# Performance work log

Hardware: AMD Instinct MI355X
Metric: run time of the kernel (lower is better)

The kernel has to match this reference:

```python
import jax, jax.numpy as jnp
import numpy as np

N_NODES = 100000
N_EDGES = 1600000
N_GRAPHS = 64
D_IN = 128
D_HID = 128
D_OUT = 4
LEAKY_SLOPE = 0.01  # nn.LeakyReLU default


def setup_inputs() -> dict:
    key = jax.random.key(0)
    k1, k2, k3, k4, k5 = jax.random.split(key, 5)
    x = jax.random.normal(k1, (N_NODES, D_IN), dtype=jnp.float32)
    edge_index = jax.random.randint(k2, (2, N_EDGES), 0, N_NODES, dtype=jnp.int32)
    batch = jnp.sort(jax.random.randint(k3, (N_NODES,), 0, N_GRAPHS, dtype=jnp.int32))
    s1 = 1.0 / np.sqrt(D_IN)
    W1 = jax.random.uniform(k4, (D_IN, D_HID), jnp.float32, -s1, s1)
    b1 = jnp.zeros((D_HID,), jnp.float32)
    W2 = jax.random.uniform(k5, (D_HID, D_OUT), jnp.float32, -s1, s1)
    b2 = jnp.zeros((D_OUT,), jnp.float32)
    return {"x": x, "edge_index": edge_index, "batch": batch,
            "W1": W1, "b1": b1, "W2": W2, "b2": b2}


def _gcn_conv(x, src, dst, norm, W, b, n_nodes):
    # h = X W; messages = norm * h[src]; aggregate at dst; add bias
    h = x @ W
    msg = h[src] * norm[:, None]
    agg = jax.ops.segment_sum(msg, dst, num_segments=n_nodes)
    return agg + b


def reference(x, edge_index, batch, W1, b1, W2, b2):
    n = x.shape[0]
    # add self-loops (PyG GCNConv default)
    loops = jnp.arange(n, dtype=edge_index.dtype)
    src = jnp.concatenate([edge_index[0], loops])
    dst = jnp.concatenate([edge_index[1], loops])
    # symmetric normalization: deg over target index, weight 1
    deg = jax.ops.segment_sum(jnp.ones_like(src, dtype=x.dtype), dst, num_segments=n)
    deg_is = jnp.where(deg > 0, jax.lax.rsqrt(deg), 0.0)
    norm = deg_is[src] * deg_is[dst]

    h = _gcn_conv(x, src, dst, norm, W1, b1, n)
    h = jnp.where(h >= 0, h, LEAKY_SLOPE * h)  # LeakyReLU
    # dropout is identity at inference
    h = _gcn_conv(h, src, dst, norm, W2, b2, n)

    # global mean pool over graphs
    sums = jax.ops.segment_sum(h, batch, num_segments=N_GRAPHS)
    cnts = jax.ops.segment_sum(jnp.ones((n,), h.dtype), batch, num_segments=N_GRAPHS)
    pooled = sums / jnp.maximum(cnts, 1.0)[:, None]
    return jax.nn.softmax(pooled, axis=1)
```

## Files before the change

### kernel.cpp

```cpp
#include <hip/hip_runtime.h>

#define D 128
#define NG 64
#define NPB 256
#define MAXBK 512
#define CAPB 8192
#define PCHUNK 4096
#define PLCAP 5376
#define ENTCAP 21
#define LDA 136

typedef unsigned int uint;
typedef unsigned short ushort_t;
typedef unsigned char uchar_t;
typedef float v2f __attribute__((ext_vector_type(2)));
typedef short s8v __attribute__((ext_vector_type(8)));
typedef float f4v __attribute__((ext_vector_type(4)));

__device__ __forceinline__ uint bfr(float x) {
    uint u = __float_as_uint(x);
    return (u + 0x7FFFu + ((u >> 16) & 1u)) >> 16;
}

__global__ __launch_bounds__(256) void k_init(const float* __restrict__ W,
                                              short* __restrict__ W1T,
                                              int* __restrict__ gcur,
                                              float* __restrict__ psum,
                                              float* __restrict__ pcnt, int NBK) {
    int tid = threadIdx.x;
    int idx = blockIdx.x * 256 + tid;
    int nn = idx >> 7, kk = idx & 127;
    W1T[idx] = (short)bfr(W[kk * D + nn]);
    if (idx < NBK) gcur[idx] = idx * CAPB;
    if (blockIdx.x == 0) {
        psum[tid] = 0.f;
        if (tid < NG) pcnt[tid] = 0.f;
    }
}

__global__ __launch_bounds__(256) void k_part(const int* __restrict__ edge,
                                              int* __restrict__ gcur, int* __restrict__ p1,
                                              int E, int NBK) {
    __shared__ int hist[MAXBK], scn[MAXBK], curb[MAXBK], fixb[MAXBK];
    __shared__ int ps[256];
    __shared__ int sortb[PCHUNK];
    __shared__ ushort_t sbkt[PCHUNK];
    int tid = threadIdx.x;
    for (int i = tid; i < MAXBK; i += 256) { hist[i] = 0; curb[i] = 0; }
    __syncthreads();
    int lo = blockIdx.x * PCHUNK;
    int hi = min(lo + PCHUNK, E);
    int cnt = hi - lo;
    for (int e = lo + tid; e < hi; e += 256) atomicAdd(&hist[edge[E + e] >> 8], 1);
    __syncthreads();
    int a = hist[2 * tid], b = hist[2 * tid + 1];
    ps[tid] = a + b;
    __syncthreads();
    for (int o = 1; o < 256; o <<= 1) {
        int x = (tid >= o) ? ps[tid - o] : 0;
        __syncthreads();
        ps[tid] += x;
        __syncthreads();
    }
    int pe = ps[tid] - (a + b);
    scn[2 * tid] = pe;
    scn[2 * tid + 1] = pe + a;
    __syncthreads();
    for (int bk = tid; bk < NBK; bk += 256)
        if (hist[bk]) fixb[bk] = atomicAdd(&gcur[bk], hist[bk]) - scn[bk];
    __syncthreads();
    for (int e = lo + tid; e < hi; e += 256) {
        int s = edge[e];
        int d2 = edge[E + e];
        int bk = d2 >> 8;
        int r = scn[bk] + atomicAdd(&curb[bk], 1);
        sortb[r] = ((d2 & 255) << 17) | s;
        sbkt[r] = (ushort_t)bk;
    }
    __syncthreads();
    for (int p = tid; p < cnt; p += 256) {
        int bk = sbkt[p];
        p1[fixb[bk] + p] = sortb[p];
    }
}

__global__ __launch_bounds__(256) void k_place(const int* __restrict__ p1,
                                               const int* __restrict__ gcur,
                                               int* __restrict__ ed, int2* __restrict__ offdeg,
                                               float* __restrict__ dinv, int n) {
    __shared__ int cnts[256], scn[256], cur[256];
    __shared__ int outb[PLCAP];
    __shared__ int tot;
    int tid = threadIdx.x;
    int b = blockIdx.x;
    int base = b * CAPB;
    int cnt = gcur[b] - base;
    int end = base + cnt;
    int node0 = b << 8;
    cnts[tid] = 0;
    cur[tid] = 0;
    __syncthreads();
    int ent[ENTCAP];
    int ne = 0;
    for (int p = base + tid; p < end; p += 256) {
        int v = p1[p];
        if (ne < ENTCAP) ent[ne] = v;
        ne++;
        atomicAdd(&cnts[v >> 17], 1);
    }
    __syncthreads();
    int v0 = cnts[tid];
    int pc = (v0 + 3) & ~3;
    scn[tid] = pc;
    __syncthreads();
    for (int o = 1; o < 256; o <<= 1) {
        int x = (tid >= o) ? scn[tid - o] : 0;
        __syncthreads();
        scn[tid] += x;
        __syncthreads();
    }
    int excl = scn[tid] - pc;
    if (tid == 255) tot = scn[255];
    int node = node0 + tid;
    if (node < n) {
        offdeg[node] = make_int2(base + excl, v0);
        dinv[node] = rsqrtf((float)(v0 + 1));
    }
    scn[tid] = excl;
    __syncthreads();
    int m = (ne < ENTCAP) ? ne : ENTCAP;
    for (int k = 0; k < m; ++k) {
        int v = ent[k];
        int l = v >> 17;
        int r = scn[l] + atomicAdd(&cur[l], 1);
        if (r < PLCAP) outb[r] = v & 0x1FFFF;
        else ed[base + r] = v & 0x1FFFF;
    }
    for (int p = base + tid + ENTCAP * 256; p < end; p += 256) {
        int v = p1[p];
        int l = v >> 17;
        int r = scn[l] + atomicAdd(&cur[l], 1);
        if (r < PLCAP) outb[r] = v & 0x1FFFF;
        else ed[base + r] = v & 0x1FFFF;
    }
    __syncthreads();
    int lim = (tot < PLCAP) ? tot : PLCAP;
    for (int p = tid; p < lim; p += 256) ed[base + p] = outb[p];
}

__global__ __launch_bounds__(256) void k_gemm_mfma(const float* __restrict__ X,
                                                   const short* __restrict__ W1T,
                                                   const float* __restrict__ dinv,
                                                   uchar_t* __restrict__ H8b, int M) {
    __shared__ short sA[128 * LDA];
    __shared__ short sB[128 * LDA];
    __shared__ float sDinv[128];
    const int tid = threadIdx.x;
    const int blockM = blockIdx.x * 128;

    if (tid < 128) {
        int gm = blockM + tid;
        sDinv[tid] = (gm < M) ? dinv[gm] : 0.f;
    }
    {
        int c = tid & 31, g = tid >> 5;
#pragma unroll
        for (int i = 0; i < 16; ++i) {
            int r = g + i * 8;
            int gm = blockM + r;
            float4 v = make_float4(0, 0, 0, 0);
            if (gm < M) v = *(const float4*)&X[(size_t)gm * D + c * 4];
            uint lo = bfr(v.x) | (bfr(v.y) << 16);
            uint hi = bfr(v.z) | (bfr(v.w) << 16);
            *(uint2*)&sA[r * LDA + c * 4] = make_uint2(lo, hi);
        }
    }
    {
        int nn = tid >> 1, seg = tid & 1;
        const short* src = W1T + nn * 128 + seg * 64;
        short* dst = &sB[nn * LDA + seg * 64];
#pragma unroll
        for (int i = 0; i < 8; ++i)
            *(int4*)&dst[i * 8] = *(const int4*)&src[i * 8];
    }
    __syncthreads();

    const int wv = tid >> 6;
    const int lane = tid & 63;
    const int m0w = (wv >> 1) * 64, n0w = (wv & 1) * 64;
    const int mrow = lane & 15;
    const int quad = lane >> 4;

    f4v acc[4][4];
#pragma unroll
    for (int mi = 0; mi < 4; ++mi)
#pragma unroll
        for (int ni = 0; ni < 4; ++ni) acc[mi][ni] = (f4v)(0.f);

#pragma unroll
    for (int ks = 0; ks < 4; ++ks) {
        s8v af[4], bf[4];
#pragma unroll
        for (int mi = 0; mi < 4; ++mi)
            af[mi] = *(const s8v*)&sA[(m0w + mi * 16 + mrow) * LDA + ks * 32 + quad * 8];
#pragma unroll
        for (int ni = 0; ni < 4; ++ni)
            bf[ni] = *(const s8v*)&sB[(n0w + ni * 16 + mrow) * LDA + ks * 32 + quad * 8];
#pragma unroll
        for (int mi = 0; mi < 4; ++mi)
#pragma unroll
            for (int ni = 0; ni < 4; ++ni)
                acc[mi][ni] = __builtin_amdgcn_mfma_f32_16x16x32_bf16(af[mi], bf[ni], acc[mi][ni], 0, 0, 0);
    }

#pragma unroll
    for (int mi = 0; mi < 4; ++mi) {
#pragma unroll
        for (int r = 0; r < 4; ++r) {
            int lrow = m0w + mi * 16 + quad * 4 + r;
            int gm = blockM + lrow;
            if (gm >= M) continue;
            float di = sDinv[lrow];
#pragma unroll
            for (int ni = 0; ni < 4; ++ni) {
                int col = n0w + ni * 16 + mrow;
                float v = acc[mi][ni][r] * di;
                uint p = __builtin_amdgcn_cvt_pk_fp8_f32(v, v, 0u, false);
                H8b[(size_t)gm * 128 + col] = (uchar_t)(p & 0xFF);
            }
        }
    }
}

__device__ __forceinline__ void acc4(float& c0, float& c1, float& c2, float& c3, uint r) {
    v2f lo = __builtin_amdgcn_cvt_pk_f32_fp8(r, false);
    v2f hi = __builtin_amdgcn_cvt_pk_f32_fp8(r, true);
    c0 += lo.x; c1 += lo.y; c2 += hi.x; c3 += hi.y;
}

__global__ __launch_bounds__(256) void k_gather(const uint* __restrict__ T,
                                                const int2* __restrict__ offdeg,
                                                const int* __restrict__ ed,
                                                const float* __restrict__ dinv,
                                                const float* __restrict__ b1,
                                                const float* __restrict__ W2,
                                                float4* __restrict__ zs,
                                                int n) {
    int tid = threadIdx.x;
    int node = blockIdx.x * 8 + (tid >> 5);
    if (node >= n) return;
    int lane = tid & 31;
    int f = lane * 4;
    float di = dinv[node];
    float c0, c1, c2, c3;
    {
        uint h = T[(node << 5) + lane];
        v2f lo = __builtin_amdgcn_cvt_pk_f32_fp8(h, false);
        v2f hi = __builtin_amdgcn_cvt_pk_f32_fp8(h, true);
        c0 = lo.x; c1 = lo.y; c2 = hi.x; c3 = hi.y;
    }
    float w[4][4], bb[4];
#pragma unroll
    for (int i = 0; i < 4; ++i) {
        bb[i] = b1[f + i];
#pragma unroll
        for (int k = 0; k < 4; ++k) w[i][k] = W2[(f + i) * 4 + k];
    }
    int2 od = offdeg[node];
    int j = od.x, j1 = od.x + od.y;
    for (; j + 8 <= j1; j += 8) {
        int4 e0 = *(const int4*)&ed[j];
        int4 e1 = *(const int4*)&ed[j + 4];
        uint r0 = T[(e0.x << 5) + lane];
        uint r1 = T[(e0.y << 5) + lane];
        uint r2 = T[(e0.z << 5) + lane];
        uint r3 = T[(e0.w << 5) + lane];
        uint r4 = T[(e1.x << 5) + lane];
        uint r5 = T[(e1.y << 5) + lane];
        uint r6 = T[(e1.z << 5) + lane];
        uint r7 = T[(e1.w << 5) + lane];
        acc4(c0, c1, c2, c3, r0); acc4(c0, c1, c2, c3, r1);
        acc4(c0, c1, c2, c3, r2); acc4(c0, c1, c2, c3, r3);
        acc4(c0, c1, c2, c3, r4); acc4(c0, c1, c2, c3, r5);
        acc4(c0, c1, c2, c3, r6); acc4(c0, c1, c2, c3, r7);
    }
    if (j + 4 <= j1) {
        int4 e0 = *(const int4*)&ed[j];
        uint r0 = T[(e0.x << 5) + lane];
        uint r1 = T[(e0.y << 5) + lane];
        uint r2 = T[(e0.z << 5) + lane];
        uint r3 = T[(e0.w << 5) + lane];
        acc4(c0, c1, c2, c3, r0); acc4(c0, c1, c2, c3, r1);
        acc4(c0, c1, c2, c3, r2); acc4(c0, c1, c2, c3, r3);
        j += 4;
    }
    for (; j < j1; ++j) {
        uint r = T[(ed[j] << 5) + lane];
        acc4(c0, c1, c2, c3, r);
    }
    float v0 = di * c0 + bb[0];
    float v1 = di * c1 + bb[1];
    float v2 = di * c2 + bb[2];
    float v3 = di * c3 + bb[3];
    v0 = v0 >= 0.f ? v0 : 0.01f * v0;
    v1 = v1 >= 0.f ? v1 : 0.01f * v1;
    v2 = v2 >= 0.f ? v2 : 0.01f * v2;
    v3 = v3 >= 0.f ? v3 : 0.01f * v3;
    float a0 = v0 * w[0][0] + v1 * w[1][0] + v2 * w[2][0] + v3 * w[3][0];
    float a1 = v0 * w[0][1] + v1 * w[1][1] + v2 * w[2][1] + v3 * w[3][1];
    float a2 = v0 * w[0][2] + v1 * w[1][2] + v2 * w[2][2] + v3 * w[3][2];
    float a3 = v0 * w[0][3] + v1 * w[1][3] + v2 * w[2][3] + v3 * w[3][3];
#pragma unroll
    for (int o = 16; o >= 1; o >>= 1) {
        a0 += __shfl_xor(a0, o);
        a1 += __shfl_xor(a1, o);
        a2 += __shfl_xor(a2, o);
        a3 += __shfl_xor(a3, o);
    }
    if (lane == 0) zs[node] = make_float4(di * a0, di * a1, di * a2, di * a3);
}

__global__ __launch_bounds__(256) void k_pool2(const int* __restrict__ p1,
                                               const int* __restrict__ gcur,
                                               const float4* __restrict__ zs,
                                               const float* __restrict__ dinv,
                                               const int* __restrict__ batch,
                                               float* __restrict__ psum, float* __restrict__ pcnt,
                                               int n) {
    __shared__ float ls[NG * 4];
    __shared__ float lc[NG];
    __shared__ float dinvd[NPB];
    __shared__ int gl[NPB];
    int tid = threadIdx.x;
    int b = blockIdx.x >> 1;
    int half = blockIdx.x & 1;
    int node0 = b << 8;
    int node = node0 + tid;
    ls[tid] = 0.f;
    if (tid < NG) lc[tid] = 0.f;
    bool valid = node < n;
    float di = valid ? dinv[node] : 0.f;
    int g = valid ? batch[node] : -1;
    dinvd[tid] = di;
    gl[tid] = g;
    __syncthreads();
    float a0 = 0.f, a1 = 0.f, a2 = 0.f, a3 = 0.f;
    int cg = -1;
    if (half == 0 && valid) {
        float4 zv = zs[node];
        cg = g;
        a0 = di * zv.x; a1 = di * zv.y; a2 = di * zv.z; a3 = di * zv.w;
        atomicAdd(&lc[g], 1.f);
    }
    int base = b * CAPB;
    int cnt = gcur[b] - base;
    int mid = cnt >> 1;
    int s0 = base + (half ? mid : 0);
    int s1 = base + (half ? cnt : mid);
    for (int p = s0 + tid; p < s1; p += 1024) {
        int vv[4];
        float4 zb[4];
        int nb = 0;
#pragma unroll
        for (int k = 0; k < 4; ++k) {
            int q = p + k * 256;
            if (q < s1) vv[nb++] = p1[q];
        }
#pragma unroll
        for (int k = 0; k < 4; ++k)
            if (k < nb) zb[k] = zs[vv[k] & 0x1FFFF];
#pragma unroll
        for (int k = 0; k < 4; ++k) {
            if (k >= nb) continue;
            int dl = vv[k] >> 17;
            float w = dinvd[dl];
            int eg = gl[dl];
            if (eg != cg) {
                if (cg >= 0) {
                    atomicAdd(&ls[cg * 4 + 0], a0);
                    atomicAdd(&ls[cg * 4 + 1], a1);
                    atomicAdd(&ls[cg * 4 + 2], a2);
                    atomicAdd(&ls[cg * 4 + 3], a3);
                }
                cg = eg;
                a0 = a1 = a2 = a3 = 0.f;
            }
            a0 += w * zb[k].x; a1 += w * zb[k].y; a2 += w * zb[k].z; a3 += w * zb[k].w;
        }
    }
    if (cg >= 0) {
        atomicAdd(&ls[cg * 4 + 0], a0);
        atomicAdd(&ls[cg * 4 + 1], a1);
        atomicAdd(&ls[cg * 4 + 2], a2);
        atomicAdd(&ls[cg * 4 + 3], a3);
    }
    __syncthreads();
    atomicAdd(&psum[tid], ls[tid]);
    if (tid < NG) atomicAdd(&pcnt[tid], lc[tid]);
}

__global__ void k_final(const float* __restrict__ psum, const float* __restrict__ pcnt,
                        const float* __restrict__ b2, float* __restrict__ out) {
    int g = threadIdx.x;
    float c = fmaxf(pcnt[g], 1.f);
    float inv = 1.f / c;
    float l0 = psum[g * 4 + 0] * inv + b2[0];
    float l1 = psum[g * 4 + 1] * inv + b2[1];
    float l2 = psum[g * 4 + 2] * inv + b2[2];
    float l3 = psum[g * 4 + 3] * inv + b2[3];
    float m = fmaxf(fmaxf(l0, l1), fmaxf(l2, l3));
    float e0 = expf(l0 - m), e1 = expf(l1 - m), e2 = expf(l2 - m), e3 = expf(l3 - m);
    float s = 1.f / (e0 + e1 + e2 + e3);
    *(float4*)&out[g * 4] = make_float4(e0 * s, e1 * s, e2 * s, e3 * s);
}

extern "C" void kernel_launch(void* const* d_in, const int* in_sizes, int n_in,
                              void* d_out, int out_size, void* d_ws, size_t ws_size,
                              hipStream_t stream) {
    const float* X = (const float*)d_in[0];
    const int* edge = (const int*)d_in[1];
    const int* batch = (const int*)d_in[2];
    const float* W1 = (const float*)d_in[3];
    const float* b1 = (const float*)d_in[4];
    const float* W2 = (const float*)d_in[5];
    const float* b2 = (const float*)d_in[6];
    float* out = (float*)d_out;
    const int n = in_sizes[2];
    const int E = in_sizes[1] / 2;
    const int NBK = (n + NPB - 1) / NPB;

    uint* Hs = (uint*)d_ws;
    int* p1 = (int*)(Hs + (size_t)n * 32);
    int* ed = p1 + (size_t)NBK * CAPB;
    float4* zs = (float4*)(ed + (size_t)NBK * CAPB);
    float* dinv = (float*)(zs + n);
    int2* offdeg = (int2*)(dinv + n);
    short* W1T = (short*)(offdeg + n);
    int* gcur = (int*)(W1T + 16384);
    float* psum = (float*)(gcur + MAXBK);
    float* pcnt = psum + NG * 4;

    const int NP = (E + PCHUNK - 1) / PCHUNK;
    const int NGB = (n + 7) / 8;

    k_init<<<64, 256, 0, stream>>>(W1, W1T, gcur, psum, pcnt, NBK);
    k_part<<<NP, 256, 0, stream>>>(edge, gcur, p1, E, NBK);
    k_place<<<NBK, 256, 0, stream>>>(p1, gcur, ed, offdeg, dinv, n);

    k_gemm_mfma<<<(n + 127) / 128, 256, 0, stream>>>(X, W1T, dinv, (uchar_t*)Hs, n);

    k_gather<<<NGB, 256, 0, stream>>>(Hs, offdeg, ed, dinv, b1, W2, zs, n);

    k_pool2<<<NBK * 2, 256, 0, stream>>>(p1, gcur, zs, dinv, batch, psum, pcnt, n);
    k_final<<<1, 64, 0, stream>>>(psum, pcnt, b2, out);
}
```

Baseline: 227.7 us.

## Vectorize edge loads and raise ILP across partition, place, gather and pool kernels

k_part now processes half-sized chunks and reads its edges as int4 vectors held in registers for both the histogram and the scatter passes. k_place runs with 512 threads, holding its whole bucket in int4 registers, which removes the ENTCAP spill path. k_gather unrolls the neighbour gather to 16 loads, loads W2 as float4 after the loop, and adds an occupancy hint to launch bounds. k_pool2 reads packed edges as int4 and aligns its split point to 4. The aim is fewer memory instructions and more loads in flight, at the cost of higher register pressure and more k_part blocks doing global atomics.

```diff
diff --git a/kernel.cpp b/kernel.cpp
--- a/kernel.cpp
+++ b/kernel.cpp
@@ -5,9 +5,8 @@
 #define NPB 256
 #define MAXBK 512
 #define CAPB 8192
-#define PCHUNK 4096
+#define PCHUNK 2048
 #define PLCAP 5376
-#define ENTCAP 21
 #define LDA 136
 
 typedef unsigned int uint;
@@ -51,7 +50,31 @@
     int lo = blockIdx.x * PCHUNK;
     int hi = min(lo + PCHUNK, E);
     int cnt = hi - lo;
-    for (int e = lo + tid; e < hi; e += 256) atomicAdd(&hist[edge[E + e] >> 8], 1);
+    int4 dv[2], sv[2];
+#pragma unroll
+    for (int it = 0; it < 2; ++it) {
+        int q = lo + tid * 4 + it * 1024;
+        if (q + 4 <= hi) {
+            dv[it] = *(const int4*)&edge[E + q];
+            sv[it] = *(const int4*)&edge[q];
+            atomicAdd(&hist[dv[it].x >> 8], 1);
+            atomicAdd(&hist[dv[it].y >> 8], 1);
+            atomicAdd(&hist[dv[it].z >> 8], 1);
+            atomicAdd(&hist[dv[it].w >> 8], 1);
+        } else {
+            dv[it].x = (q + 0 < hi) ? edge[E + q + 0] : 0;
+            dv[it].y = (q + 1 < hi) ? edge[E + q + 1] : 0;
+            dv[it].z = (q + 2 < hi) ? edge[E + q + 2] : 0;
+            dv[it].w = 0;
+            sv[it].x = (q + 0 < hi) ? edge[q + 0] : 0;
+            sv[it].y = (q + 1 < hi) ? edge[q + 1] : 0;
+            sv[it].z = (q + 2 < hi) ? edge[q + 2] : 0;
+            sv[it].w = 0;
+            if (q + 0 < hi) atomicAdd(&hist[dv[it].x >> 8], 1);
+            if (q + 1 < hi) atomicAdd(&hist[dv[it].y >> 8], 1);
+            if (q + 2 < hi) atomicAdd(&hist[dv[it].z >> 8], 1);
+        }
+    }
     __syncthreads();
     int a = hist[2 * tid], b = hist[2 * tid + 1];
     ps[tid] = a + b;
@@ -69,13 +92,45 @@
     for (int bk = tid; bk < NBK; bk += 256)
         if (hist[bk]) fixb[bk] = atomicAdd(&gcur[bk], hist[bk]) - scn[bk];
     __syncthreads();
-    for (int e = lo + tid; e < hi; e += 256) {
-        int s = edge[e];
-        int d2 = edge[E + e];
-        int bk = d2 >> 8;
-        int r = scn[bk] + atomicAdd(&curb[bk], 1);
-        sortb[r] = ((d2 & 255) << 17) | s;
-        sbkt[r] = (ushort_t)bk;
+#pragma unroll
+    for (int it = 0; it < 2; ++it) {
+        int q = lo + tid * 4 + it * 1024;
+        {
+            int d2 = dv[it].x, s = sv[it].x;
+            if (q + 0 < hi) {
+                int bk = d2 >> 8;
+                int r = scn[bk] + atomicAdd(&curb[bk], 1);
+                sortb[r] = ((d2 & 255) << 17) | s;
+                sbkt[r] = (ushort_t)bk;
+            }
+        }
+        {
+            int d2 = dv[it].y, s = sv[it].y;
+            if (q + 1 < hi) {
+                int bk = d2 >> 8;
+                int r = scn[bk] + atomicAdd(&curb[bk], 1);
+                sortb[r] = ((d2 & 255) << 17) | s;
+                sbkt[r] = (ushort_t)bk;
+            }
+        }
+        {
+            int d2 = dv[it].z, s = sv[it].z;
+            if (q + 2 < hi) {
+                int bk = d2 >> 8;
+                int r = scn[bk] + atomicAdd(&curb[bk], 1);
+                sortb[r] = ((d2 & 255) << 17) | s;
+                sbkt[r] = (ushort_t)bk;
+            }
+        }
+        {
+            int d2 = dv[it].w, s = sv[it].w;
+            if (q + 3 < hi) {
+                int bk = d2 >> 8;
+                int r = scn[bk] + atomicAdd(&curb[bk], 1);
+                sortb[r] = ((d2 & 255) << 17) | s;
+                sbkt[r] = (ushort_t)bk;
+            }
+        }
     }
     __syncthreads();
     for (int p = tid; p < cnt; p += 256) {
@@ -84,7 +139,7 @@
     }
 }
 
-__global__ __launch_bounds__(256) void k_place(const int* __restrict__ p1,
+__global__ __launch_bounds__(512) void k_place(const int* __restrict__ p1,
                                                const int* __restrict__ gcur,
                                                int* __restrict__ ed, int2* __restrict__ offdeg,
                                                float* __restrict__ dinv, int n) {
@@ -97,55 +152,90 @@
     int cnt = gcur[b] - base;
     int end = base + cnt;
     int node0 = b << 8;
-    cnts[tid] = 0;
-    cur[tid] = 0;
-    __syncthreads();
-    int ent[ENTCAP];
-    int ne = 0;
-    for (int p = base + tid; p < end; p += 256) {
-        int v = p1[p];
-        if (ne < ENTCAP) ent[ne] = v;
-        ne++;
-        atomicAdd(&cnts[v >> 17], 1);
-    }
-    __syncthreads();
-    int v0 = cnts[tid];
-    int pc = (v0 + 3) & ~3;
-    scn[tid] = pc;
+    if (tid < 256) { cnts[tid] = 0; cur[tid] = 0; }
+    __syncthreads();
+    int4 ev[4];
+#pragma unroll
+    for (int it = 0; it < 4; ++it) {
+        int q = base + tid * 4 + it * 2048;
+        ev[it] = *(const int4*)&p1[q];
+        if (q + 4 <= end) {
+            atomicAdd(&cnts[ev[it].x >> 17], 1);
+            atomicAdd(&cnts[ev[it].y >> 17], 1);
+            atomicAdd(&cnts[ev[it].z >> 17], 1);
+            atomicAdd(&cnts[ev[it].w >> 17], 1);
+        } else if (q < end) {
+            atomicAdd(&cnts[ev[it].x >> 17], 1);
+            if (q + 1 < end) atomicAdd(&cnts[ev[it].y >> 17], 1);
+            if (q + 2 < end) atomicAdd(&cnts[ev[it].z >> 17], 1);
+        }
+    }
+    __syncthreads();
+    int v0 = 0, pc = 0;
+    if (tid < 256) {
+        v0 = cnts[tid];
+        pc = (v0 + 3) & ~3;
+        scn[tid] = pc;
+    }
     __syncthreads();
     for (int o = 1; o < 256; o <<= 1) {
-        int x = (tid >= o) ? scn[tid - o] : 0;
+        int x = 0;
+        if (tid < 256 && tid >= o) x = scn[tid - o];
         __syncthreads();
-        scn[tid] += x;
+        if (tid < 256) scn[tid] += x;
         __syncthreads();
     }
-    int excl = scn[tid] - pc;
     if (tid == 255) tot = scn[255];
-    int node = node0 + tid;
-    if (node < n) {
-        offdeg[node] = make_int2(base + excl, v0);
-        dinv[node] = rsqrtf((float)(v0 + 1));
-    }
-    scn[tid] = excl;
-    __syncthreads();
-    int m = (ne < ENTCAP) ? ne : ENTCAP;
-    for (int k = 0; k < m; ++k) {
-        int v = ent[k];
-        int l = v >> 17;
-        int r = scn[l] + atomicAdd(&cur[l], 1);
-        if (r < PLCAP) outb[r] = v & 0x1FFFF;
-        else ed[base + r] = v & 0x1FFFF;
-    }
-    for (int p = base + tid + ENTCAP * 256; p < end; p += 256) {
-        int v = p1[p];
-        int l = v >> 17;
-        int r = scn[l] + atomicAdd(&cur[l], 1);
-        if (r < PLCAP) outb[r] = v & 0x1FFFF;
-        else ed[base + r] = v & 0x1FFFF;
+    if (tid < 256) {
+        int excl = scn[tid] - pc;
+        int node = node0 + tid;
+        if (node < n) {
+            offdeg[node] = make_int2(base + excl, v0);
+            dinv[node] = rsqrtf((float)(v0 + 1));
+        }
+    }
+    __syncthreads();
+    if (tid < 256) scn[tid] -= pc;
+    __syncthreads();
+#pragma unroll
+    for (int it = 0; it < 4; ++it) {
+        int q = base + tid * 4 + it * 2048;
+        {
+            int v = ev[it].x;
+            if (q + 0 < end) {
+                int l = v >> 17;
+                int r = scn[l] + atomicAdd(&cur[l], 1);
+                if (r < PLCAP) outb[r] = v & 0x1FFFF; else ed[base + r] = v & 0x1FFFF;
+            }
+        }
+        {
+            int v = ev[it].y;
+            if (q + 1 < end) {
+                int l = v >> 17;
+                int r = scn[l] + atomicAdd(&cur[l], 1);
+                if (r < PLCAP) outb[r] = v & 0x1FFFF; else ed[base + r] = v & 0x1FFFF;
+            }
+        }
+        {
+            int v = ev[it].z;
+            if (q + 2 < end) {
+                int l = v >> 17;
+                int r = scn[l] + atomicAdd(&cur[l], 1);
+                if (r < PLCAP) outb[r] = v & 0x1FFFF; else ed[base + r] = v & 0x1FFFF;
+            }
+        }
+        {
+            int v = ev[it].w;
+            if (q + 3 < end) {
+                int l = v >> 17;
+                int r = scn[l] + atomicAdd(&cur[l], 1);
+                if (r < PLCAP) outb[r] = v & 0x1FFFF; else ed[base + r] = v & 0x1FFFF;
+            }
+        }
     }
     __syncthreads();
     int lim = (tot < PLCAP) ? tot : PLCAP;
-    for (int p = tid; p < lim; p += 256) ed[base + p] = outb[p];
+    for (int p = tid; p < lim; p += 512) ed[base + p] = outb[p];
 }
 
 __global__ __launch_bounds__(256) void k_gemm_mfma(const float* __restrict__ X,
@@ -238,78 +328,84 @@
     c0 += lo.x; c1 += lo.y; c2 += hi.x; c3 += hi.y;
 }
 
-__global__ __launch_bounds__(256) void k_gather(const uint* __restrict__ T,
-                                                const int2* __restrict__ offdeg,
-                                                const int* __restrict__ ed,
-                                                const float* __restrict__ dinv,
-                                                const float* __restrict__ b1,
-                                                const float* __restrict__ W2,
-                                                float4* __restrict__ zs,
-                                                int n) {
+__global__ __launch_bounds__(256, 8) void k_gather(const uint* __restrict__ T,
+                                                   const int2* __restrict__ offdeg,
+                                                   const int* __restrict__ ed,
+                                                   const float* __restrict__ dinv,
+                                                   const float* __restrict__ b1,
+                                                   const float* __restrict__ W2,
+                                                   float4* __restrict__ zs,
+                                                   int n) {
     int tid = threadIdx.x;
     int node = blockIdx.x * 8 + (tid >> 5);
     if (node >= n) return;
     int lane = tid & 31;
-    int f = lane * 4;
+    const uint* Tl = T + lane;
     float di = dinv[node];
     float c0, c1, c2, c3;
     {
-        uint h = T[(node << 5) + lane];
+        uint h = Tl[node << 5];
         v2f lo = __builtin_amdgcn_cvt_pk_f32_fp8(h, false);
         v2f hi = __builtin_amdgcn_cvt_pk_f32_fp8(h, true);
         c0 = lo.x; c1 = lo.y; c2 = hi.x; c3 = hi.y;
     }
-    float w[4][4], bb[4];
-#pragma unroll
-    for (int i = 0; i < 4; ++i) {
-        bb[i] = b1[f + i];
-#pragma unroll
-        for (int k = 0; k < 4; ++k) w[i][k] = W2[(f + i) * 4 + k];
-    }
     int2 od = offdeg[node];
     int j = od.x, j1 = od.x + od.y;
-    for (; j + 8 <= j1; j += 8) {
+    for (; j + 16 <= j1; j += 16) {
         int4 e0 = *(const int4*)&ed[j];
         int4 e1 = *(const int4*)&ed[j + 4];
-        uint r0 = T[(e0.x << 5) + lane];
-        uint r1 = T[(e0.y << 5) + lane];
-        uint r2 = T[(e0.z << 5) + lane];
-        uint r3 = T[(e0.w << 5) + lane];
-        uint r4 = T[(e1.x << 5) + lane];
-        uint r5 = T[(e1.y << 5) + lane];
-        uint r6 = T[(e1.z << 5) + lane];
-        uint r7 = T[(e1.w << 5) + lane];
+        int4 e2 = *(const int4*)&ed[j + 8];
+        int4 e3 = *(const int4*)&ed[j + 12];
+        uint r0 = Tl[e0.x << 5], r1 = Tl[e0.y << 5], r2 = Tl[e0.z << 5], r3 = Tl[e0.w << 5];
+        uint r4 = Tl[e1.x << 5], r5 = Tl[e1.y << 5], r6 = Tl[e1.z << 5], r7 = Tl[e1.w << 5];
+        uint r8 = Tl[e2.x << 5], r9 = Tl[e2.y << 5], r10 = Tl[e2.z << 5], r11 = Tl[e2.w << 5];
+        uint r12 = Tl[e3.x << 5], r13 = Tl[e3.y << 5], r14 = Tl[e3.z << 5], r15 = Tl[e3.w << 5];
+        acc4(c0, c1, c2, c3, r0);  acc4(c0, c1, c2, c3, r1);
+        acc4(c0, c1, c2, c3, r2);  acc4(c0, c1, c2, c3, r3);
+        acc4(c0, c1, c2, c3, r4);  acc4(c0, c1, c2, c3, r5);
+        acc4(c0, c1, c2, c3, r6);  acc4(c0, c1, c2, c3, r7);
+        acc4(c0, c1, c2, c3, r8);  acc4(c0, c1, c2, c3, r9);
+        acc4(c0, c1, c2, c3, r10); acc4(c0, c1, c2, c3, r11);
+        acc4(c0, c1, c2, c3, r12); acc4(c0, c1, c2, c3, r13);
+        acc4(c0, c1, c2, c3, r14); acc4(c0, c1, c2, c3, r15);
+    }
+    if (j + 8 <= j1) {
+        int4 e0 = *(const int4*)&ed[j];
+        int4 e1 = *(const int4*)&ed[j + 4];
+        uint r0 = Tl[e0.x << 5], r1 = Tl[e0.y << 5], r2 = Tl[e0.z << 5], r3 = Tl[e0.w << 5];
+        uint r4 = Tl[e1.x << 5], r5 = Tl[e1.y << 5], r6 = Tl[e1.z << 5], r7 = Tl[e1.w << 5];
         acc4(c0, c1, c2, c3, r0); acc4(c0, c1, c2, c3, r1);
         acc4(c0, c1, c2, c3, r2); acc4(c0, c1, c2, c3, r3);
         acc4(c0, c1, c2, c3, r4); acc4(c0, c1, c2, c3, r5);
         acc4(c0, c1, c2, c3, r6); acc4(c0, c1, c2, c3, r7);
+        j += 8;
     }
     if (j + 4 <= j1) {
         int4 e0 = *(const int4*)&ed[j];
-        uint r0 = T[(e0.x << 5) + lane];
-        uint r1 = T[(e0.y << 5) + lane];
-        uint r2 = T[(e0.z << 5) + lane];
-        uint r3 = T[(e0.w << 5) + lane];
+        uint r0 = Tl[e0.x << 5], r1 = Tl[e0.y << 5], r2 = Tl[e0.z << 5], r3 = Tl[e0.w << 5];
         acc4(c0, c1, c2, c3, r0); acc4(c0, c1, c2, c3, r1);
         acc4(c0, c1, c2, c3, r2); acc4(c0, c1, c2, c3, r3);
         j += 4;
     }
     for (; j < j1; ++j) {
-        uint r = T[(ed[j] << 5) + lane];
+        uint r = Tl[ed[j] << 5];
         acc4(c0, c1, c2, c3, r);
     }
-    float v0 = di * c0 + bb[0];
-    float v1 = di * c1 + bb[1];
-    float v2 = di * c2 + bb[2];
-    float v3 = di * c3 + bb[3];
+    int f = lane * 4;
+    float v0 = di * c0 + b1[f + 0];
+    float v1 = di * c1 + b1[f + 1];
+    float v2 = di * c2 + b1[f + 2];
+    float v3 = di * c3 + b1[f + 3];
     v0 = v0 >= 0.f ? v0 : 0.01f * v0;
     v1 = v1 >= 0.f ? v1 : 0.01f * v1;
     v2 = v2 >= 0.f ? v2 : 0.01f * v2;
     v3 = v3 >= 0.f ? v3 : 0.01f * v3;
-    float a0 = v0 * w[0][0] + v1 * w[1][0] + v2 * w[2][0] + v3 * w[3][0];
-    float a1 = v0 * w[0][1] + v1 * w[1][1] + v2 * w[2][1] + v3 * w[3][1];
-    float a2 = v0 * w[0][2] + v1 * w[1][2] + v2 * w[2][2] + v3 * w[3][2];
-    float a3 = v0 * w[0][3] + v1 * w[1][3] + v2 * w[2][3] + v3 * w[3][3];
+    const float4* W2v = (const float4*)W2;
+    float4 w0 = W2v[f + 0], w1 = W2v[f + 1], w2 = W2v[f + 2], w3 = W2v[f + 3];
+    float a0 = v0 * w0.x + v1 * w1.x + v2 * w2.x + v3 * w3.x;
+    float a1 = v0 * w0.y + v1 * w1.y + v2 * w2.y + v3 * w3.y;
+    float a2 = v0 * w0.z + v1 * w1.z + v2 * w2.z + v3 * w3.z;
+    float a3 = v0 * w0.w + v1 * w1.w + v2 * w2.w + v3 * w3.w;
 #pragma unroll
     for (int o = 16; o >= 1; o >>= 1) {
         a0 += __shfl_xor(a0, o);
@@ -346,6 +442,22 @@
     __syncthreads();
     float a0 = 0.f, a1 = 0.f, a2 = 0.f, a3 = 0.f;
     int cg = -1;
+    auto PROC = [&](int v, float4 zv) {
+        int dl = v >> 17;
+        float w = dinvd[dl];
+        int eg = gl[dl];
+        if (eg != cg) {
+            if (cg >= 0) {
+                atomicAdd(&ls[cg * 4 + 0], a0);
+                atomicAdd(&ls[cg * 4 + 1], a1);
+                atomicAdd(&ls[cg * 4 + 2], a2);
+                atomicAdd(&ls[cg * 4 + 3], a3);
+            }
+            cg = eg;
+            a0 = a1 = a2 = a3 = 0.f;
+        }
+        a0 += w * zv.x; a1 += w * zv.y; a2 += w * zv.z; a3 += w * zv.w;
+    };
     if (half == 0 && valid) {
         float4 zv = zs[node];
         cg = g;
@@ -354,39 +466,21 @@
     }
     int base = b * CAPB;
     int cnt = gcur[b] - base;
-    int mid = cnt >> 1;
+    int mid = (cnt >> 1) & ~3;
     int s0 = base + (half ? mid : 0);
     int s1 = base + (half ? cnt : mid);
-    for (int p = s0 + tid; p < s1; p += 1024) {
-        int vv[4];
-        float4 zb[4];
-        int nb = 0;
-#pragma unroll
-        for (int k = 0; k < 4; ++k) {
-            int q = p + k * 256;
-            if (q < s1) vv[nb++] = p1[q];
-        }
-#pragma unroll
-        for (int k = 0; k < 4; ++k)
-            if (k < nb) zb[k] = zs[vv[k] & 0x1FFFF];
-#pragma unroll
-        for (int k = 0; k < 4; ++k) {
-            if (k >= nb) continue;
-            int dl = vv[k] >> 17;
-            float w = dinvd[dl];
-            int eg = gl[dl];
-            if (eg != cg) {
-                if (cg >= 0) {
-                    atomicAdd(&ls[cg * 4 + 0], a0);
-                    atomicAdd(&ls[cg * 4 + 1], a1);
-                    atomicAdd(&ls[cg * 4 + 2], a2);
-                    atomicAdd(&ls[cg * 4 + 3], a3);
-                }
-                cg = eg;
-                a0 = a1 = a2 = a3 = 0.f;
-            }
-            a0 += w * zb[k].x; a1 += w * zb[k].y; a2 += w * zb[k].z; a3 += w * zb[k].w;
-        }
+    int p0 = s0 + tid * 4;
+    for (; p0 + 4 <= s1; p0 += 1024) {
+        int4 vv = *(const int4*)&p1[p0];
+        float4 zb0 = zs[vv.x & 0x1FFFF];
+        float4 zb1 = zs[vv.y & 0x1FFFF];
+        float4 zb2 = zs[vv.z & 0x1FFFF];
+        float4 zb3 = zs[vv.w & 0x1FFFF];
+        PROC(vv.x, zb0); PROC(vv.y, zb1); PROC(vv.z, zb2); PROC(vv.w, zb3);
+    }
+    for (; p0 < s1; ++p0) {
+        int v = p1[p0];
+        PROC(v, zs[v & 0x1FFFF]);
     }
     if (cg >= 0) {
         atomicAdd(&ls[cg * 4 + 0], a0);
@@ -445,7 +539,7 @@
 
     k_init<<<64, 256, 0, stream>>>(W1, W1T, gcur, psum, pcnt, NBK);
     k_part<<<NP, 256, 0, stream>>>(edge, gcur, p1, E, NBK);
-    k_place<<<NBK, 256, 0, stream>>>(p1, gcur, ed, offdeg, dinv, n);
+    k_place<<<NBK, 512, 0, stream>>>(p1, gcur, ed, offdeg, dinv, n);
 
     k_gemm_mfma<<<(n + 127) / 128, 256, 0, stream>>>(X, W1T, dinv, (uchar_t*)Hs, n);
 
```

New measurement: 224.9 us (median of 2 runs). Within noise of the previous version (-1.2%).
